# Kernel optimization log

Measured on AMD Instinct MI355X. Metric: run time of the kernel, lower is better.

Reference implementation:

```python
import jax, jax.numpy as jnp
import numpy as np

B, N, D, L = 16, 100, 1024, 2000


def setup_inputs() -> dict:
    key = jax.random.key(0)
    ks = jax.random.split(key, 9)
    s = 1.0 / np.sqrt(D)
    return {
        "feature": jax.random.normal(ks[0], (B, N, D), dtype=jnp.float32),
        "graph": jax.random.randint(ks[1], (B, N, N), 0, L),
        "W0": jax.random.normal(ks[2], (D, D), dtype=jnp.float32) * s,
        "W1": jax.random.normal(ks[3], (D, D), dtype=jnp.float32) * s,
        "bias": jax.random.uniform(ks[4], (L, D), dtype=jnp.float32, minval=-s, maxval=s),
        "dp_Wa": jax.random.normal(ks[5], (D, D), dtype=jnp.float32) * s,
        "dp_ba": jax.random.normal(ks[6], (D,), dtype=jnp.float32) * s,
        "dp_Wb": jax.random.normal(ks[7], (D, D), dtype=jnp.float32) * s,
        "dp_bb": jax.random.normal(ks[8], (D,), dtype=jnp.float32) * s,
        "get_alpha": 0,
    }


def reference(feature, graph, W0, W1, bias, dp_Wa, dp_ba, dp_Wb, dp_bb, get_alpha):
    # ---- DirectedGraphConv.conv ----
    adj = (graph != 0).astype(feature.dtype)                     # [B,N,N]
    out = feature + feature @ W0.T + feature @ W1.T              # [B,N,D]
    out = out + jnp.take(bias, graph, axis=0).sum(axis=2)        # label-embedding gather+sum over neighbors
    # ---- relation_alpha: DotProduct(feature, feature) ----
    a = feature @ dp_Wa.T + dp_ba                                # [B,N,D]
    b = feature @ dp_Wb.T + dp_bb                                # [B,N,D]
    alpha = jnp.einsum('bik,bjk->bij', a, b)                     # [B,N,N]
    alpha = jnp.maximum(alpha, 0.0)                              # alpha[alpha<0]=0
    alpha = jnp.einsum('bij,bjk->bik', adj, alpha)               # bmm(adj, alpha)
    alpha = jax.nn.softmax(alpha, axis=1)                        # Softmax(dim=1)
    out = jnp.einsum('bij,bjk->bik', alpha, out)                 # bmm(alpha, output)
    if get_alpha:
        return (out, alpha)
    return out
```

## Files before the change

kernel.cpp:

```cpp
#include <hip/hip_runtime.h>
#include <stdint.h>

#define B_   16
#define N_   100
#define D_   1024
#define L_   2000
#define M_   1600
#define KP   2048
#define AK   3072

#define RCAP 24
#define DCAP 32
#define ZMAX 2400
#define TC   6

typedef __bf16 bf16x8 __attribute__((ext_vector_type(8)));
typedef float  f32x4  __attribute__((ext_vector_type(4)));

__device__ __forceinline__ void gl_lds16(const __bf16* g, __bf16* l) {
    __builtin_amdgcn_global_load_lds(
        (const __attribute__((address_space(1))) void*)g,
        (__attribute__((address_space(3))) void*)l, 16, 0, 0);
}


__global__ void __launch_bounds__(256)
k_prep(const float* __restrict__ f,
       const float* __restrict__ W0, const float* __restrict__ W1,
       const float* __restrict__ Wa, const float* __restrict__ Wb,
       const float* __restrict__ bias, const int* __restrict__ graph,
       __bf16* __restrict__ Acat, __bf16* __restrict__ B0cat,
       __bf16* __restrict__ wcat12, int* __restrict__ colZ) {
    int bid = blockIdx.x, t = threadIdx.x;
    __shared__ float lds[32][33];
    __shared__ unsigned int hist[KP];

    if (bid < 2336) {
        int i = bid * 256 + t;
        union { __bf16 h[8]; uint4 u; } pk;
        if (i < 204800) {
            long base = (long)i * 8;
            const float4* p = (const float4*)(f + base);
            float4 x = p[0], y = p[1];
            pk.h[0]=(__bf16)x.x; pk.h[1]=(__bf16)x.y; pk.h[2]=(__bf16)x.z; pk.h[3]=(__bf16)x.w;
            pk.h[4]=(__bf16)y.x; pk.h[5]=(__bf16)y.y; pk.h[6]=(__bf16)y.z; pk.h[7]=(__bf16)y.w;
            int m = i >> 7, c = i & 127;
            ((uint4*)Acat)[(long)m * 384 + c] = pk.u;
        } else {
            int j = i - 204800;
            long base = (long)j * 8;
            long seg = base >> 20;
            int  js  = j & 131071;
            if (seg == 0) {
                long off = (long)js * 8;
                const float4* p0 = (const float4*)(W0 + off);
                const float4* p1 = (const float4*)(W1 + off);
                float4 a0 = p0[0], a1 = p0[1], b0 = p1[0], b1 = p1[1];
                pk.h[0]=(__bf16)(a0.x+b0.x); pk.h[1]=(__bf16)(a0.y+b0.y);
                pk.h[2]=(__bf16)(a0.z+b0.z); pk.h[3]=(__bf16)(a0.w+b0.w);
                pk.h[4]=(__bf16)(a1.x+b1.x); pk.h[5]=(__bf16)(a1.y+b1.y);
                pk.h[6]=(__bf16)(a1.z+b1.z); pk.h[7]=(__bf16)(a1.w+b1.w);
                int row = js >> 7, c = js & 127;
                ((uint4*)B0cat)[(long)row * 384 + c] = pk.u;
            } else {
                const float* src = (seg == 1) ? Wa : Wb;
                long off = (long)js * 8;
                const float4* p = (const float4*)(src + off);
                float4 x = p[0], y = p[1];
                pk.h[0]=(__bf16)x.x; pk.h[1]=(__bf16)x.y; pk.h[2]=(__bf16)x.z; pk.h[3]=(__bf16)x.w;
                pk.h[4]=(__bf16)y.x; pk.h[5]=(__bf16)y.y; pk.h[6]=(__bf16)y.z; pk.h[7]=(__bf16)y.w;
                ((uint4*)wcat12)[(long)(seg - 1) * 131072 + js] = pk.u;
            }
        }
    } else if (bid < 4384) {
        int tb = bid - 2336;
        int lt = tb >> 5, dt = tb & 31;
        int l0 = lt * 32, d0 = dt * 32;
        int r = t >> 3, cq = (t & 7) * 4;
        float4 v = make_float4(0.f, 0.f, 0.f, 0.f);
        if (l0 + r < L_) v = *(const float4*)(bias + (long)(l0 + r) * D_ + d0 + cq);
        lds[r][cq]=v.x; lds[r][cq+1]=v.y; lds[r][cq+2]=v.z; lds[r][cq+3]=v.w;
        __syncthreads();
        union { __bf16 h[4]; uint2 u; } pk;
        #pragma unroll
        for (int q = 0; q < 4; ++q) pk.h[q] = (__bf16)lds[cq + q][r];
        *(uint2*)(B0cat + (long)(d0 + r) * AK + 1024 + l0 + cq) = pk.u;
    } else {
        int m = bid - 4384;
        for (int k = t; k < KP; k += 256) hist[k] = 0u;
        __syncthreads();
        if (t < N_) {
            int gv = graph[(long)m * N_ + t];
            atomicAdd(&hist[gv], 1u);
            if (gv == 0) atomicAdd(&colZ[(m / N_) * N_ + t], 1);
        }
        __syncthreads();
        union { __bf16 h[8]; uint4 u; } pk;
        #pragma unroll
        for (int q = 0; q < 8; ++q) pk.h[q] = (__bf16)(float)hist[t * 8 + q];
        ((uint4*)(Acat + (long)m * AK + 1024))[t] = pk.u;
    }
}


#define BM 64
#define BN 128
#define BK 64

__global__ void __launch_bounds__(256)
k_gemmAll(const __bf16* __restrict__ Acat, const __bf16* __restrict__ B0cat,
          const __bf16* __restrict__ wcat12, const int* __restrict__ colZ,
          const float* __restrict__ feat, const float* __restrict__ ba,
          const float* __restrict__ bbias,
          float* __restrict__ out0, float* __restrict__ bB, float* __restrict__ aD) {
    __shared__ __align__(16) __bf16 As[BM * BK];
    __shared__ __align__(16) __bf16 Bs[BN * BK];
    __shared__ int czL[2 * N_];
    __shared__ int dcolL[2][DCAP];
    int t = threadIdx.x;
    int pid = blockIdx.x;
    int lane = t & 63, wave = t >> 6;
    int wr = wave & 1, wc = wave >> 1;
    int lrow = lane & 15, quad = lane >> 4;

    int kind = (pid < 200) ? 0 : (pid < 400 ? 1 : 2);
    int bm, bn, K;
    long ldb;
    const __bf16 *Bg;
    if (kind == 0) {
        bn = pid & 7; bm = pid >> 3;
        Bg = B0cat + (long)(bn * BN) * AK;
        ldb = AK; K = AK;
    } else if (kind == 1) {
        int p2 = pid - 200;
        bn = p2 & 7; bm = p2 >> 3;
        Bg = wcat12 + (long)(1024 + bn * BN) * 1024;
        ldb = 1024; K = 1024;
    } else {
        int p3 = pid - 400;
        bn = p3 & 7; bm = p3 >> 3;
        Bg = wcat12 + (long)(bn * BN) * 1024;
        ldb = 1024; K = 1024;
        if (t < 2 * N_) czL[t] = colZ[bm * 2 * N_ + t];
        __syncthreads();
        if (t < 2) {
            int rank = 0;
            for (int j = 0; j < N_; ++j)
                if (czL[t * N_ + j] > 0 && rank < DCAP) dcolL[t][rank++] = j;
            for (; rank < DCAP; ++rank) dcolL[t][rank] = 0;
        }
        __syncthreads();
    }

    int r0 = t >> 3, r1 = 32 + (t >> 3);
    int c0 = (t & 7) ^ (r0 & 7), c1 = (t & 7) ^ (r1 & 7);
    const __bf16 *aS0, *aS1;
    if (kind == 2) {
        int b0g = bm * 2 + (r0 >> 5), s0 = r0 & 31;
        int b1g = bm * 2 + (r1 >> 5), s1 = r1 & 31;
        aS0 = Acat + (long)(b0g * N_ + dcolL[r0 >> 5][s0]) * AK + c0 * 8;
        aS1 = Acat + (long)(b1g * N_ + dcolL[r1 >> 5][s1]) * AK + c1 * 8;
    } else {
        aS0 = Acat + (long)(bm * BM + r0) * AK + c0 * 8;
        aS1 = Acat + (long)(bm * BM + r1) * AK + c1 * 8;
    }
    const __bf16 *bS[4];
    #pragma unroll
    for (int pi = 0; pi < 4; ++pi) {
        int rb = pi * 32 + (t >> 3), cb = (t & 7) ^ (rb & 7);
        bS[pi] = Bg + (long)rb * ldb + cb * 8;
    }

    f32x4 acc[2][4] = {};
    for (int k0 = 0; k0 < K; k0 += BK) {
        gl_lds16(aS0 + k0, As + t * 8);
        gl_lds16(aS1 + k0, As + (256 + t) * 8);
        #pragma unroll
        for (int pi = 0; pi < 4; ++pi)
            gl_lds16(bS[pi] + k0, Bs + (pi * 256 + t) * 8);
        __syncthreads();
        #pragma unroll
        for (int ks = 0; ks < 2; ++ks) {
            bf16x8 af[2], bf[4];
            #pragma unroll
            for (int i = 0; i < 2; ++i) {
                int r = wr * 32 + i * 16 + lrow;
                int slot = r * 8 + (((ks << 2) | quad) ^ (r & 7));
                af[i] = *(const bf16x8*)(As + slot * 8);
            }
            #pragma unroll
            for (int j = 0; j < 4; ++j) {
                int r = wc * 64 + j * 16 + lrow;
                int slot = r * 8 + (((ks << 2) | quad) ^ (r & 7));
                bf[j] = *(const bf16x8*)(Bs + slot * 8);
            }
            #pragma unroll
            for (int i = 0; i < 2; ++i)
                #pragma unroll
                for (int j = 0; j < 4; ++j)
                    acc[i][j] = __builtin_amdgcn_mfma_f32_16x16x32_bf16(af[i], bf[j], acc[i][j], 0, 0, 0);
        }
        __syncthreads();
    }

    #pragma unroll
    for (int i = 0; i < 2; ++i) {
        int gm0 = bm * BM + wr * 32 + i * 16 + quad * 4;
        #pragma unroll
        for (int j = 0; j < 4; ++j) {
            int col = bn * BN + wc * 64 + j * 16 + lrow;
            #pragma unroll
            for (int r = 0; r < 4; ++r) {
                long m = gm0 + r;
                float v = acc[i][j][r];
                if (kind == 0)      out0[m * D_ + col] = v + feat[m * D_ + col];
                else if (kind == 1) bB[m * D_ + col]   = v + bbias[col];
                else                aD[m * D_ + col]   = v + ba[col];
            }
        }
    }
}


__global__ void __launch_bounds__(256)
k_alpha(const int* __restrict__ graph, const __bf16* __restrict__ Acat,
        const int* __restrict__ colZ, const float* __restrict__ aD,
        const float* __restrict__ bB, float* __restrict__ wl, float* __restrict__ cwG) {
    __shared__ int rowCnt[N_], rowOff[N_], rowRank[N_];
    __shared__ int czA[N_], colSlotL[N_];
    __shared__ int ndvS, totZS;
    __shared__ int zjL[ZMAX];
    __shared__ short prL[ZMAX];
    __shared__ float corrL[RCAP][4];
    __shared__ float wred[4][4];

    int pid = blockIdx.x;
    int b = pid / 25, kc = pid - b * 25;
    int t = threadIdx.x, lane = t & 63, wave = t >> 6;

    const int* g = graph + (long)b * N_ * N_;
    if (t < N_) {
        rowCnt[t] = (int)(float)Acat[(long)(b * N_ + t) * AK + 1024];
        czA[t] = colZ[b * N_ + t];
    }
    if (t < RCAP * 4) corrL[t >> 2][t & 3] = 0.f;
    __syncthreads();
    if (t == 0) {
        int off = 0, rank = 0;
        for (int i = 0; i < N_; ++i) {
            if (rowCnt[i] > 0 && rank < RCAP) {
                rowRank[i] = rank; rowOff[i] = off; off += rowCnt[i]; ++rank;
            } else rowRank[i] = -1;
        }
        ndvS = rank; totZS = off;
    }
    if (t == 64) {
        int ds = 0;
        for (int j = 0; j < N_; ++j) {
            if (czA[j] > 0) { colSlotL[j] = (ds < DCAP) ? ds : 0; ++ds; }
            else colSlotL[j] = -1;
        }
    }
    __syncthreads();
    if (t < N_ && rowRank[t] >= 0) {
        int pos = rowOff[t], r = rowRank[t];
        for (int j = 0; j < N_; ++j)
            if (g[t * N_ + j] == 0) { zjL[pos] = j; prL[pos] = (short)r; ++pos; }
    }
    __syncthreads();
    int Z = totZS, ndv = ndvS;

    int k0 = kc * 4;
    float4 bv[4];
    #pragma unroll
    for (int kk = 0; kk < 4; ++kk)
        bv[kk] = *(const float4*)(bB + ((long)(b * N_ + k0 + kk)) * D_ + t * 4);

    for (int q = 0; q < Z; ++q) {
        int slot = colSlotL[zjL[q]];
        const float* ar = aD + ((long)(b * DCAP + slot)) * D_;
        float4 av = *(const float4*)(ar + t * 4);
        float s[4];
        #pragma unroll
        for (int kk = 0; kk < 4; ++kk)
            s[kk] = av.x * bv[kk].x + av.y * bv[kk].y + av.z * bv[kk].z + av.w * bv[kk].w;
        #pragma unroll
        for (int off = 32; off > 0; off >>= 1)
            #pragma unroll
            for (int kk = 0; kk < 4; ++kk) s[kk] += __shfl_xor(s[kk], off);
        if (lane == 0) { wred[wave][0]=s[0]; wred[wave][1]=s[1]; wred[wave][2]=s[2]; wred[wave][3]=s[3]; }
        __syncthreads();
        if (t < 4) {
            float v = wred[0][t] + wred[1][t] + wred[2][t] + wred[3][t];
            corrL[prL[q]][t] += fmaxf(v, 0.f);
        }
        __syncthreads();
    }

    if (t < 4) {
        int k = k0 + t;
        float denom = (float)(N_ - ndv);
        for (int r = 0; r < ndv; ++r) {
            float e = __expf(-corrL[r][t]);
            corrL[r][t] = e;
            denom += e;
        }
        float w = 1.f / denom;
        wl[b * N_ + k] = w;
        for (int r = 0; r < ndv; ++r)
            cwG[((long)b * RCAP + r) * N_ + k] = corrL[r][t] * w;
    }
}


__global__ void __launch_bounds__(256)
k_mix(const __bf16* __restrict__ Acat, const float* __restrict__ wl,
      const float* __restrict__ cwG, const float* __restrict__ out0,
      float* __restrict__ out) {
    int b = blockIdx.x, dq = blockIdx.y;
    int t = threadIdx.x, c4 = t & 31, q = t >> 5;
    int d0 = dq * 128;
    __shared__ int hasZ[N_], mapL[N_], ndvS;
    __shared__ float wT[TC][N_];
    __shared__ f32x4 parts[8][TC][32];

    if (t < N_)
        hasZ[t] = ((float)Acat[(long)(b * N_ + t) * AK + 1024] > 0.f) ? 1 : 0;
    __syncthreads();
    if (t < N_) {
        int rank = 0;
        for (int i = 0; i < t; ++i) rank += hasZ[i];
        mapL[t] = (hasZ[t] && rank < RCAP) ? 1 + rank : 0;
    }
    if (t == 0) {
        int n = 0;
        for (int i = 0; i < N_; ++i) n += hasZ[i];
        ndvS = min(n, RCAP);
    }
    __syncthreads();
    int ndv = ndvS, ntask = ndv + 1;

    const float* o0 = out0 + (long)b * N_ * D_ + d0;
    for (int cb = 0; cb < ntask; cb += TC) {
        for (int idx = t; idx < TC * N_; idx += 256) {
            int rr = idx / N_, j = idx - rr * N_;
            int task = cb + rr;
            float v = 0.f;
            if (task == 0)         v = wl[b * N_ + j];
            else if (task <= ndv)  v = cwG[((long)b * RCAP + task - 1) * N_ + j];
            wT[rr][j] = v;
        }
        __syncthreads();
        f32x4 acc[TC] = {};
        for (int j = q; j < N_; j += 8) {
            f32x4 v = *(const f32x4*)(o0 + (long)j * D_ + c4 * 4);
            #pragma unroll
            for (int rr = 0; rr < TC; ++rr) acc[rr] += wT[rr][j] * v;
        }
        #pragma unroll
        for (int rr = 0; rr < TC; ++rr) parts[q][rr][c4] = acc[rr];
        __syncthreads();
        for (int i = q; i < N_; i += 8) {
            int task = mapL[i];
            if (task >= cb && task < cb + TC) {
                int rr = task - cb;
                f32x4 s = parts[0][rr][c4];
                #pragma unroll
                for (int p = 1; p < 8; ++p) s += parts[p][rr][c4];
                *(f32x4*)(out + ((long)(b * N_ + i)) * D_ + d0 + c4 * 4) = s;
            }
        }
        __syncthreads();
    }
}


extern "C" void kernel_launch(void* const* d_in, const int* in_sizes, int n_in,
                              void* d_out, int out_size, void* d_ws, size_t ws_size,
                              hipStream_t stream) {
    const float* feature = (const float*)d_in[0];
    const int*   graph   = (const int*)d_in[1];
    const float* W0      = (const float*)d_in[2];
    const float* W1      = (const float*)d_in[3];
    const float* bias    = (const float*)d_in[4];
    const float* dp_Wa   = (const float*)d_in[5];
    const float* dp_ba   = (const float*)d_in[6];
    const float* dp_Wb   = (const float*)d_in[7];
    const float* dp_bb   = (const float*)d_in[8];
    float* out = (float*)d_out;

    char* w = (char*)d_ws;
    __bf16* Acat   = (__bf16*)(w);
    __bf16* B0cat  = (__bf16*)(w + 9830400);
    __bf16* wcat12 = (__bf16*)(w + 16121856);
    float*  out0   = (float*)(w + 20316160);
    float*  bB     = (float*)(w + 26869760);
    float*  aD     = (float*)(w + 33423360);
    float*  wl     = (float*)(w + 35520512);
    float*  cwG    = (float*)(w + 35526912);
    int*    colZ   = (int*)  (w + 35680512);

    hipMemsetAsync(colZ, 0, B_ * N_ * sizeof(int), stream);
    k_prep<<<5984, 256, 0, stream>>>(feature, W0, W1, dp_Wa, dp_Wb, bias, graph,
                                     Acat, B0cat, wcat12, colZ);
    k_gemmAll<<<464, 256, 0, stream>>>(Acat, B0cat, wcat12, colZ, feature, dp_ba, dp_bb,
                                       out0, bB, aD);
    k_alpha<<<400, 256, 0, stream>>>(graph, Acat, colZ, aD, bB, wl, cwG);
    k_mix<<<dim3(B_, 8), 256, 0, stream>>>(Acat, wl, cwG, out0, out);
}
```

Measured before the change: 183.5 us.

## Split long-K GEMM into three K-chunks, sum partials in mix kernel

```diff
diff --git a/kernel.cpp b/kernel.cpp
--- a/kernel.cpp
+++ b/kernel.cpp
@@ -85,20 +85,24 @@
         #pragma unroll
         for (int q = 0; q < 4; ++q) pk.h[q] = (__bf16)lds[cq + q][r];
         *(uint2*)(B0cat + (long)(d0 + r) * AK + 1024 + l0 + cq) = pk.u;
-    } else {
+    } else if (bid < 5984) {
         int m = bid - 4384;
         for (int k = t; k < KP; k += 256) hist[k] = 0u;
         __syncthreads();
-        if (t < N_) {
-            int gv = graph[(long)m * N_ + t];
-            atomicAdd(&hist[gv], 1u);
-            if (gv == 0) atomicAdd(&colZ[(m / N_) * N_ + t], 1);
-        }
+        if (t < N_) atomicAdd(&hist[graph[(long)m * N_ + t]], 1u);
         __syncthreads();
         union { __bf16 h[8]; uint4 u; } pk;
         #pragma unroll
         for (int q = 0; q < 8; ++q) pk.h[q] = (__bf16)(float)hist[t * 8 + q];
         ((uint4*)(Acat + (long)m * AK + 1024))[t] = pk.u;
+    } else {
+        int b = bid - 5984;
+        if (t < N_) {
+            const int* g = graph + (long)b * N_ * N_;
+            int c = 0;
+            for (int i = 0; i < N_; ++i) c += (g[i * N_ + t] == 0);
+            colZ[b * N_ + t] = c;
+        }
     }
 }
 
@@ -112,7 +116,8 @@
           const __bf16* __restrict__ wcat12, const int* __restrict__ colZ,
           const float* __restrict__ feat, const float* __restrict__ ba,
           const float* __restrict__ bbias,
-          float* __restrict__ out0, float* __restrict__ bB, float* __restrict__ aD) {
+          float* __restrict__ out0, float* __restrict__ out0b, float* __restrict__ out0c,
+          float* __restrict__ bB, float* __restrict__ aD) {
     __shared__ __align__(16) __bf16 As[BM * BK];
     __shared__ __align__(16) __bf16 Bs[BN * BK];
     __shared__ int czL[2 * N_];
@@ -123,24 +128,30 @@
     int wr = wave & 1, wc = wave >> 1;
     int lrow = lane & 15, quad = lane >> 4;
 
-    int kind = (pid < 200) ? 0 : (pid < 400 ? 1 : 2);
-    int bm, bn, K;
-    long ldb;
+    int kind, chunk = 0, bm, bn;
+    long ldb, koff = 0;
     const __bf16 *Bg;
-    if (kind == 0) {
-        bn = pid & 7; bm = pid >> 3;
-        Bg = B0cat + (long)(bn * BN) * AK;
-        ldb = AK; K = AK;
-    } else if (kind == 1) {
-        int p2 = pid - 200;
-        bn = p2 & 7; bm = p2 >> 3;
+    if (pid < 600) {
+        kind = 0; chunk = pid / 200;
+        int p = pid - chunk * 200;
+        int v = (p & 7) * 25 + (p >> 3);
+        bm = v >> 3; bn = v & 7;
+        koff = (long)chunk * 1024;
+        Bg = B0cat + (long)(bn * BN) * AK + koff;
+        ldb = AK;
+    } else if (pid < 800) {
+        kind = 1;
+        int p = pid - 600;
+        int v = (p & 7) * 25 + (p >> 3);
+        bm = v >> 3; bn = v & 7;
         Bg = wcat12 + (long)(1024 + bn * BN) * 1024;
-        ldb = 1024; K = 1024;
+        ldb = 1024;
     } else {
-        int p3 = pid - 400;
-        bn = p3 & 7; bm = p3 >> 3;
+        kind = 2;
+        int p = pid - 800;
+        bn = p & 7; bm = p >> 3;
         Bg = wcat12 + (long)(bn * BN) * 1024;
-        ldb = 1024; K = 1024;
+        ldb = 1024;
         if (t < 2 * N_) czL[t] = colZ[bm * 2 * N_ + t];
         __syncthreads();
         if (t < 2) {
@@ -161,8 +172,8 @@
         aS0 = Acat + (long)(b0g * N_ + dcolL[r0 >> 5][s0]) * AK + c0 * 8;
         aS1 = Acat + (long)(b1g * N_ + dcolL[r1 >> 5][s1]) * AK + c1 * 8;
     } else {
-        aS0 = Acat + (long)(bm * BM + r0) * AK + c0 * 8;
-        aS1 = Acat + (long)(bm * BM + r1) * AK + c1 * 8;
+        aS0 = Acat + (long)(bm * BM + r0) * AK + koff + c0 * 8;
+        aS1 = Acat + (long)(bm * BM + r1) * AK + koff + c1 * 8;
     }
     const __bf16 *bS[4];
     #pragma unroll
@@ -172,7 +183,7 @@
     }
 
     f32x4 acc[2][4] = {};
-    for (int k0 = 0; k0 < K; k0 += BK) {
+    for (int k0 = 0; k0 < 1024; k0 += BK) {
         gl_lds16(aS0 + k0, As + t * 8);
         gl_lds16(aS1 + k0, As + (256 + t) * 8);
         #pragma unroll
@@ -213,9 +224,12 @@
             for (int r = 0; r < 4; ++r) {
                 long m = gm0 + r;
                 float v = acc[i][j][r];
-                if (kind == 0)      out0[m * D_ + col] = v + feat[m * D_ + col];
-                else if (kind == 1) bB[m * D_ + col]   = v + bbias[col];
-                else                aD[m * D_ + col]   = v + ba[col];
+                if (kind == 0) {
+                    if (chunk == 0)      out0[m * D_ + col]  = v + feat[m * D_ + col];
+                    else if (chunk == 1) out0b[m * D_ + col] = v;
+                    else                 out0c[m * D_ + col] = v;
+                } else if (kind == 1) bB[m * D_ + col] = v + bbias[col];
+                else                  aD[m * D_ + col] = v + ba[col];
             }
         }
     }
@@ -316,13 +330,14 @@
 __global__ void __launch_bounds__(256)
 k_mix(const __bf16* __restrict__ Acat, const float* __restrict__ wl,
       const float* __restrict__ cwG, const float* __restrict__ out0,
+      const float* __restrict__ out0b, const float* __restrict__ out0c,
       float* __restrict__ out) {
     int b = blockIdx.x, dq = blockIdx.y;
-    int t = threadIdx.x, c4 = t & 31, q = t >> 5;
-    int d0 = dq * 128;
+    int t = threadIdx.x, c4 = t & 15, q = t >> 4;
+    int d0 = dq * 64;
     __shared__ int hasZ[N_], mapL[N_], ndvS;
     __shared__ float wT[TC][N_];
-    __shared__ f32x4 parts[8][TC][32];
+    __shared__ f32x4 parts[16][TC][16];
 
     if (t < N_)
         hasZ[t] = ((float)Acat[(long)(b * N_ + t) * AK + 1024] > 0.f) ? 1 : 0;
@@ -340,7 +355,9 @@
     __syncthreads();
     int ndv = ndvS, ntask = ndv + 1;
 
-    const float* o0 = out0 + (long)b * N_ * D_ + d0;
+    const float* o0 = out0  + (long)b * N_ * D_ + d0;
+    const float* ob = out0b + (long)b * N_ * D_ + d0;
+    const float* oc = out0c + (long)b * N_ * D_ + d0;
     for (int cb = 0; cb < ntask; cb += TC) {
         for (int idx = t; idx < TC * N_; idx += 256) {
             int rr = idx / N_, j = idx - rr * N_;
@@ -352,21 +369,23 @@
         }
         __syncthreads();
         f32x4 acc[TC] = {};
-        for (int j = q; j < N_; j += 8) {
-            f32x4 v = *(const f32x4*)(o0 + (long)j * D_ + c4 * 4);
+        for (int j = q; j < N_; j += 16) {
+            f32x4 v = *(const f32x4*)(o0 + (long)j * D_ + c4 * 4)
+                    + *(const f32x4*)(ob + (long)j * D_ + c4 * 4)
+                    + *(const f32x4*)(oc + (long)j * D_ + c4 * 4);
             #pragma unroll
             for (int rr = 0; rr < TC; ++rr) acc[rr] += wT[rr][j] * v;
         }
         #pragma unroll
         for (int rr = 0; rr < TC; ++rr) parts[q][rr][c4] = acc[rr];
         __syncthreads();
-        for (int i = q; i < N_; i += 8) {
+        for (int i = q; i < N_; i += 16) {
             int task = mapL[i];
             if (task >= cb && task < cb + TC) {
                 int rr = task - cb;
                 f32x4 s = parts[0][rr][c4];
                 #pragma unroll
-                for (int p = 1; p < 8; ++p) s += parts[p][rr][c4];
+                for (int p = 1; p < 16; ++p) s += parts[p][rr][c4];
                 *(f32x4*)(out + ((long)(b * N_ + i)) * D_ + d0 + c4 * 4) = s;
             }
         }
@@ -394,17 +413,18 @@
     __bf16* B0cat  = (__bf16*)(w + 9830400);
     __bf16* wcat12 = (__bf16*)(w + 16121856);
     float*  out0   = (float*)(w + 20316160);
-    float*  bB     = (float*)(w + 26869760);
-    float*  aD     = (float*)(w + 33423360);
-    float*  wl     = (float*)(w + 35520512);
-    float*  cwG    = (float*)(w + 35526912);
-    int*    colZ   = (int*)  (w + 35680512);
-
-    hipMemsetAsync(colZ, 0, B_ * N_ * sizeof(int), stream);
-    k_prep<<<5984, 256, 0, stream>>>(feature, W0, W1, dp_Wa, dp_Wb, bias, graph,
+    float*  out0b  = (float*)(w + 26869760);
+    float*  out0c  = (float*)(w + 33423360);
+    float*  bB     = (float*)(w + 39976960);
+    float*  aD     = (float*)(w + 46530560);
+    float*  wl     = (float*)(w + 48627712);
+    float*  cwG    = (float*)(w + 48634112);
+    int*    colZ   = (int*)  (w + 48787712);
+
+    k_prep<<<6000, 256, 0, stream>>>(feature, W0, W1, dp_Wa, dp_Wb, bias, graph,
                                      Acat, B0cat, wcat12, colZ);
-    k_gemmAll<<<464, 256, 0, stream>>>(Acat, B0cat, wcat12, colZ, feature, dp_ba, dp_bb,
-                                       out0, bB, aD);
+    k_gemmAll<<<864, 256, 0, stream>>>(Acat, B0cat, wcat12, colZ, feature, dp_ba, dp_bb,
+                                       out0, out0b, out0c, bB, aD);
     k_alpha<<<400, 256, 0, stream>>>(graph, Acat, colZ, aD, bB, wl, cwG);
-    k_mix<<<dim3(B_, 8), 256, 0, stream>>>(Acat, wl, cwG, out0, out);
-}
+    k_mix<<<dim3(B_, 16), 256, 0, stream>>>(Acat, wl, cwG, out0, out0b, out0c, out);
+}
```

New measurement: 163.8 us (median of 2 runs). 10.7% less time.
